# Kernel tuning notes

Hardware: AMD Instinct MI355X
Metric: run time of the kernel (lower is better)

Reference implementation:

```python
import jax, jax.numpy as jnp
import numpy as np

EPS = 1e-8
NUM_HEADS = 4


def setup_inputs() -> dict:
    key = jax.random.key(0)
    ks = jax.random.split(key, 20)
    N, D = 8192, 200      # total nodes, gnn/text dim
    B = 4                  # graphs (text batch)
    E, DEG = 4096, 16      # hyperedges, nodes per hyperedge
    H = 128                # fusion hidden dim
    f = lambda k, s: jax.random.normal(k, s, dtype=jnp.float32) * 0.05
    return {
        "x": jax.random.normal(ks[0], (N, D), dtype=jnp.float32),
        "text": jax.random.normal(ks[1], (B, D), dtype=jnp.float32),
        "W": f(ks[2], (D, D)),
        "b": jnp.zeros((D,), jnp.float32),
        "gate_w": f(ks[3], (D, 1)),
        "gate_b": jnp.zeros((1,), jnp.float32),
        "gnn_w": f(ks[4], (D, H)), "gnn_b": f(ks[5], (H,)),
        "text_w": f(ks[6], (D, H)), "text_b": f(ks[7], (H,)),
        "in_w": f(ks[8], (H, 3 * H)), "in_b": f(ks[9], (3 * H,)),
        "attn_out_w": f(ks[10], (H, H)), "attn_out_b": f(ks[11], (H,)),
        "fgate_w": f(ks[12], (2 * H, H)), "fgate_b": f(ks[13], (H,)),
        "outp_w": f(ks[14], (H, D)), "outp_b": f(ks[15], (D,)),
        "edge_nodes": jax.random.randint(ks[16], (E, DEG), 0, N),
    }


def _forward(x, text, W, b, gate_w, gate_b, gnn_w, gnn_b, text_w, text_b,
             in_w, in_b, attn_out_w, attn_out_b, fgate_w, fgate_b,
             outp_w, outp_b, edge_nodes):
    N, D = x.shape
    E, DEG = edge_nodes.shape
    # --- HypergraphConv: incidence build + normalized Laplacian propagation ---
    out = x @ W                                         # [N, D]
    # H[node, edge] = 1/len(edge); duplicates overwrite (set), as in torch loop
    Hinc = jnp.zeros((N, E), x.dtype).at[edge_nodes, jnp.arange(E)[:, None]].set(1.0 / DEG)
    Dv = Hinc.sum(axis=1)                               # node degree [N]
    De = Hinc.sum(axis=0)                               # edge degree [E]
    dv = 1.0 / jnp.sqrt(Dv + EPS)
    de = 1.0 / (De + EPS)
    Hl = Hinc * dv[:, None]                             # Dv^-1/2 H
    L = (Hl * de[None, :]) @ Hl.T                       # Dv^-1/2 H De^-1 H^T Dv^-1/2
    hyper_out = L @ out                                 # [N, D]
    alpha = jax.nn.sigmoid(x.mean(axis=0, keepdims=True) @ gate_w + gate_b)  # [1,1]
    gnn_feat = alpha * out + (1.0 - alpha) * hyper_out + b
    # --- CrossModalAttentionFusion on per-graph node features (3D path) ---
    B = text.shape[0]
    Nn = N // B
    gnn3 = gnn_feat.reshape(B, Nn, D)
    gp = gnn3 @ gnn_w + gnn_b                           # [B, Nn, H]
    tp = (text @ text_w + text_b)[:, None, :]           # [B, 1, H]
    Hd = gp.shape[-1]
    hd = Hd // NUM_HEADS
    q = gp @ in_w[:, :Hd] + in_b[:Hd]
    k = tp @ in_w[:, Hd:2 * Hd] + in_b[Hd:2 * Hd]
    v = tp @ in_w[:, 2 * Hd:] + in_b[2 * Hd:]
    qh = q.reshape(B, Nn, NUM_HEADS, hd).transpose(0, 2, 1, 3)   # [B,h,Nn,hd]
    kh = k.reshape(B, 1, NUM_HEADS, hd).transpose(0, 2, 1, 3)    # [B,h,1,hd]
    vh = v.reshape(B, 1, NUM_HEADS, hd).transpose(0, 2, 1, 3)
    scores = jnp.einsum("bhqd,bhkd->bhqk", qh, kh) / jnp.sqrt(jnp.float32(hd))
    attn = jax.nn.softmax(scores, axis=-1)              # kv_len=1 -> ones
    att = jnp.einsum("bhqk,bhkd->bhqd", attn, vh)
    att = att.transpose(0, 2, 1, 3).reshape(B, Nn, Hd) @ attn_out_w + attn_out_b
    g = jax.nn.sigmoid(jnp.concatenate([gp, att], axis=-1) @ fgate_w + fgate_b)
    fused = g * gp + (1.0 - g) * att
    return fused @ outp_w + outp_b                      # [B, Nn, D]


def reference(x, text, W, b, gate_w, gate_b, gnn_w, gnn_b, text_w, text_b,
              in_w, in_b, attn_out_w, attn_out_b, fgate_w, fgate_b,
              outp_w, outp_b, edge_nodes):
    return _forward(x, text, W, b, gate_w, gate_b, gnn_w, gnn_b, text_w, text_b,
                    in_w, in_b, attn_out_w, attn_out_b, fgate_w, fgate_b,
                    outp_w, outp_b, edge_nodes)
```

## Files before the change

kernel.cpp:

```cpp
#include <hip/hip_runtime.h>
#include <hip/hip_bf16.h>

#define NODES 8192
#define DIM   200
#define NEDGE 4096
#define DEGREE 16
#define NB    4
#define NNODE 2048
#define HD    128
#define MT    8

__global__ void k_front(const float* __restrict__ x, const int* __restrict__ en,
                        const float* __restrict__ W, const float* __restrict__ gnn_w,
                        const float* __restrict__ bias, const float* __restrict__ gnn_b,
                        const float* __restrict__ text, const float* __restrict__ text_w,
                        const float* __restrict__ text_b, const float* __restrict__ in_w,
                        const float* __restrict__ in_b, const float* __restrict__ aow,
                        const float* __restrict__ aob, const float* __restrict__ fgw,
                        const float* __restrict__ fgb, float* __restrict__ colsum,
                        int* __restrict__ cnt, int* __restrict__ emask,
                        float* __restrict__ Wg, float* __restrict__ bg,
                        float* __restrict__ attO, float* __restrict__ attg) {
    __shared__ float st[DIM];
    __shared__ float part[2][HD];
    __shared__ float vin[HD];
    int b = blockIdx.x, t = threadIdx.x;
    if (b < 256) {
        if (t < DIM) {
            float acc = 0.f;
            int r0 = b * 32;
            for (int r = 0; r < 32; r++) acc += x[(r0 + r) * DIM + t];
            atomicAdd(&colsum[t], acc);
        }
        return;
    }
    if (b < 272) {
        int e = (b - 256) * 256 + t;
        int idx[DEGREE];
#pragma unroll
        for (int i = 0; i < DEGREE; i++) idx[i] = en[e * DEGREE + i];
        int mask = 0;
#pragma unroll
        for (int i = 0; i < DEGREE; i++) {
            bool uniq = true;
            for (int j = 0; j < i; j++) uniq = uniq && (idx[j] != idx[i]);
            if (uniq) { mask |= (1 << i); atomicAdd(&cnt[idx[i]], 1); }
        }
        emask[e] = mask;
        return;
    }
    if (b < 372) {
        int r = 2 * (b - 272) + (t >> 7);
        int c = t & 127;
        const float* vec = &W[r * DIM];
        float acc = 0.f;
        for (int k = 0; k < DIM; k++) acc += vec[k] * gnn_w[k * HD + c];
        Wg[r * HD + c] = acc;
        return;
    }
    if (b == 372) {
        if (t < HD) {
            float acc = 0.f;
            for (int k = 0; k < DIM; k++) acc += bias[k] * gnn_w[k * HD + t];
            bg[t] = acc + gnn_b[t];
        }
        return;
    }
    int g = b - 373;
    int c = t & 127, h = t >> 7;
    if (t < DIM) st[t] = text[g * DIM + t];
    __syncthreads();
    {
        float acc = 0.f;
        int k0 = h * 100;
        for (int k = k0; k < k0 + 100; k++) acc += st[k] * text_w[k * HD + c];
        part[h][c] = acc;
    }
    __syncthreads();
    if (t < HD) vin[t] = part[0][t] + part[1][t] + text_b[t];
    __syncthreads();
    {
        float acc = 0.f;
        int k0 = h * 64;
        for (int k = k0; k < k0 + 64; k++) acc += vin[k] * in_w[k * 3 * HD + 2 * HD + c];
        part[h][c] = acc;
    }
    __syncthreads();
    if (t < HD) vin[t] = part[0][t] + part[1][t] + in_b[2 * HD + t];
    __syncthreads();
    {
        float acc = 0.f;
        int k0 = h * 64;
        for (int k = k0; k < k0 + 64; k++) acc += vin[k] * aow[k * HD + c];
        part[h][c] = acc;
    }
    __syncthreads();
    if (t < HD) {
        float ao = part[0][t] + part[1][t] + aob[t];
        attO[g * HD + t] = ao;
        vin[t] = ao;
    }
    __syncthreads();
    {
        float acc = 0.f;
        int k0 = h * 64;
        for (int k = k0; k < k0 + 64; k++) acc += vin[k] * fgw[(HD + k) * HD + c];
        part[h][c] = acc;
    }
    __syncthreads();
    if (t < HD) attg[g * HD + t] = part[0][t] + part[1][t] + fgb[t];
}

__global__ void k_xwg(const float* __restrict__ x, const float* __restrict__ Wg,
                      float* __restrict__ out2, const float* __restrict__ colsum,
                      const float* __restrict__ gate_w, const float* __restrict__ gate_b,
                      float* __restrict__ alpha, const int* __restrict__ cnt,
                      float* __restrict__ dv) {
    __shared__ float sx[MT * DIM];
    int t = threadIdx.x;
    if (blockIdx.x == NODES / MT) {
        __shared__ float red[256];
        red[t] = (t < DIM) ? colsum[t] * gate_w[t] : 0.f;
        __syncthreads();
        for (int o = 128; o > 0; o >>= 1) {
            if (t < o) red[t] += red[t + o];
            __syncthreads();
        }
        if (t == 0) {
            float z = red[0] / (float)NODES + gate_b[0];
            alpha[0] = 1.0f / (1.0f + expf(-z));
        }
        return;
    }
    if (blockIdx.x > NODES / MT) {
        int n = (blockIdx.x - NODES / MT - 1) * 256 + t;
        dv[n] = 1.0f / sqrtf((float)cnt[n] * (1.0f / 16.0f) + 1e-8f);
        return;
    }
    int bm = blockIdx.x * MT;
    const float4* x4 = (const float4*)(x + bm * DIM);
    float4* sx4 = (float4*)sx;
    for (int i = t; i < MT * DIM / 4; i += 256) sx4[i] = x4[i];
    __syncthreads();
    int c = t & 127, rg = t >> 7;
    float acc[4] = {0.f, 0.f, 0.f, 0.f};
    for (int k = 0; k < DIM; k++) {
        float w = Wg[k * HD + c];
#pragma unroll
        for (int i = 0; i < 4; i++) acc[i] += sx[(rg * 4 + i) * DIM + k] * w;
    }
#pragma unroll
    for (int i = 0; i < 4; i++) out2[(bm + rg * 4 + i) * HD + c] = acc[i];
}

__global__ void k_edge(const int* __restrict__ en, const int* __restrict__ emask,
                       const float* __restrict__ dv, const float* __restrict__ out2,
                       float* __restrict__ accum) {
    int e = blockIdx.x * 2 + (threadIdx.x >> 7);
    int c = threadIdx.x & 127;
    int m = emask[e];
    float De = (float)__popc(m) * (1.0f / 16.0f);
    float de = 1.0f / (De + 1e-8f);
    int nd[DEGREE];
#pragma unroll
    for (int i = 0; i < DEGREE; i++) nd[i] = en[e * DEGREE + i];
    float acc = 0.f;
#pragma unroll
    for (int i = 0; i < DEGREE; i++)
        if ((m >> i) & 1) acc += dv[nd[i]] * out2[nd[i] * HD + c];
    float s = de * acc;
#pragma unroll
    for (int i = 0; i < DEGREE; i++)
        if ((m >> i) & 1) atomicAdd(&accum[nd[i] * HD + c], s);
}

__global__ void k_tail(const float* __restrict__ out2, const float* __restrict__ accum,
                       const float* __restrict__ dv, const float* __restrict__ alpha,
                       const float* __restrict__ bg, const float* __restrict__ fgw,
                       const float* __restrict__ attO, const float* __restrict__ attg,
                       const float* __restrict__ opw, const float* __restrict__ opb,
                       float* __restrict__ out) {
    __shared__ float sgp[MT][HD];
    int bm = blockIdx.x * MT;
    int b = bm >> 11;
    int t = threadIdx.x;
    int c = t & 127, rg = t >> 7;
    float a = alpha[0];
    float bgc = bg[c];
#pragma unroll
    for (int i = 0; i < 4; i++) {
        int r = rg * 4 + i;
        int n = bm + r;
        float hyp = accum[n * HD + c] * dv[n] * (1.0f / 256.0f);
        sgp[r][c] = a * out2[n * HD + c] + (1.0f - a) * hyp + bgc;
    }
    __syncthreads();
    float ao = attO[b * HD + c];
    float ag = attg[b * HD + c];
    float acc[4] = {ag, ag, ag, ag};
    for (int j = 0; j < HD; j++) {
        float w = fgw[j * HD + c];
#pragma unroll
        for (int i = 0; i < 4; i++) acc[i] += sgp[rg * 4 + i][j] * w;
    }
    __syncthreads();
#pragma unroll
    for (int i = 0; i < 4; i++) {
        int r = rg * 4 + i;
        float g = 1.0f / (1.0f + expf(-acc[i]));
        sgp[r][c] = g * sgp[r][c] + (1.0f - g) * ao;
    }
    __syncthreads();
    if (t < DIM) {
        float accO[MT];
        float ob = opb[t];
#pragma unroll
        for (int i = 0; i < MT; i++) accO[i] = ob;
        for (int j = 0; j < HD; j++) {
            float w = opw[j * DIM + t];
#pragma unroll
            for (int i = 0; i < MT; i++) accO[i] += sgp[i][j] * w;
        }
#pragma unroll
        for (int i = 0; i < MT; i++) out[(bm + i) * DIM + t] = accO[i];
    }
}

extern "C" void kernel_launch(void* const* d_in, const int* in_sizes, int n_in,
                              void* d_out, int out_size, void* d_ws, size_t ws_size,
                              hipStream_t stream) {
    const float* x      = (const float*)d_in[0];
    const float* text   = (const float*)d_in[1];
    const float* W      = (const float*)d_in[2];
    const float* bias   = (const float*)d_in[3];
    const float* gate_w = (const float*)d_in[4];
    const float* gate_b = (const float*)d_in[5];
    const float* gnn_w  = (const float*)d_in[6];
    const float* gnn_b  = (const float*)d_in[7];
    const float* text_w = (const float*)d_in[8];
    const float* text_b = (const float*)d_in[9];
    const float* in_w   = (const float*)d_in[10];
    const float* in_b   = (const float*)d_in[11];
    const float* aow    = (const float*)d_in[12];
    const float* aob    = (const float*)d_in[13];
    const float* fgw    = (const float*)d_in[14];
    const float* fgb    = (const float*)d_in[15];
    const float* opw    = (const float*)d_in[16];
    const float* opb    = (const float*)d_in[17];
    const int*   en     = (const int*)d_in[18];
    float* out = (float*)d_out;

    char* p = (char*)d_ws;
    int*   cnt    = (int*)p;   p += NODES * sizeof(int);
    float* colsum = (float*)p; p += DIM * sizeof(float);
    float* accum  = (float*)p; p += (size_t)NODES * HD * sizeof(float);
    float* out2   = (float*)p; p += (size_t)NODES * HD * sizeof(float);
    float* Wg     = (float*)p; p += DIM * HD * sizeof(float);
    float* dv     = (float*)p; p += NODES * sizeof(float);
    float* alpha  = (float*)p; p += sizeof(float);
    float* bg     = (float*)p; p += HD * sizeof(float);
    float* attO   = (float*)p; p += NB * HD * sizeof(float);
    float* attg   = (float*)p; p += NB * HD * sizeof(float);
    int*   emask  = (int*)p;   p += NEDGE * sizeof(int);

    hipMemsetAsync(cnt, 0, (NODES + DIM + NODES * HD) * sizeof(int), stream);

    k_front<<<377, 256, 0, stream>>>(x, en, W, gnn_w, bias, gnn_b, text, text_w,
                                     text_b, in_w, in_b, aow, aob, fgw, fgb,
                                     colsum, cnt, emask, Wg, bg, attO, attg);
    k_xwg<<<NODES / MT + 1 + NODES / 256, 256, 0, stream>>>(x, Wg, out2, colsum, gate_w,
                                                            gate_b, alpha, cnt, dv);
    k_edge<<<NEDGE / 2, 256, 0, stream>>>(en, emask, dv, out2, accum);
    k_tail<<<NODES / MT, 256, 0, stream>>>(out2, accum, dv, alpha, bg, fgw,
                                           attO, attg, opw, opb, out);
}
```

Before: 185.4 us.

## Replace scatter atomics with per-node edge lists and gather in tail kernel

Builds a per-node list of incident hyperedges (capped at 32) during the uniqueness pass, then stores per-edge sums to a tE buffer instead of atomically scattering into a node accumulator. The tail kernel gathers edge sums per node through this list, and the dv array is recomputed inline from counts. This removes the large memset of accum and the float atomics in the edge kernel, at the cost of an indirect gather. Nodes with more than 32 incident edges would be silently truncated, and the order in which slots are filled by atomics is nondeterministic.

```diff
diff --git a/kernel.cpp b/kernel.cpp
--- a/kernel.cpp
+++ b/kernel.cpp
@@ -9,6 +9,11 @@
 #define NNODE 2048
 #define HD    128
 #define MT    8
+#define ECAP  32
+
+__device__ __forceinline__ float dv_of(int cnt) {
+    return 1.0f / sqrtf((float)cnt * (1.0f / 16.0f) + 1e-8f);
+}
 
 __global__ void k_front(const float* __restrict__ x, const int* __restrict__ en,
                         const float* __restrict__ W, const float* __restrict__ gnn_w,
@@ -19,8 +24,9 @@
                         const float* __restrict__ aob, const float* __restrict__ fgw,
                         const float* __restrict__ fgb, float* __restrict__ colsum,
                         int* __restrict__ cnt, int* __restrict__ emask,
-                        float* __restrict__ Wg, float* __restrict__ bg,
-                        float* __restrict__ attO, float* __restrict__ attg) {
+                        int* __restrict__ elist2, float* __restrict__ Wg,
+                        float* __restrict__ bg, float* __restrict__ attO,
+                        float* __restrict__ attg) {
     __shared__ float st[DIM];
     __shared__ float part[2][HD];
     __shared__ float vin[HD];
@@ -44,7 +50,11 @@
         for (int i = 0; i < DEGREE; i++) {
             bool uniq = true;
             for (int j = 0; j < i; j++) uniq = uniq && (idx[j] != idx[i]);
-            if (uniq) { mask |= (1 << i); atomicAdd(&cnt[idx[i]], 1); }
+            if (uniq) {
+                mask |= (1 << i);
+                int slot = atomicAdd(&cnt[idx[i]], 1);
+                if (slot < ECAP) elist2[idx[i] * ECAP + slot] = e;
+            }
         }
         emask[e] = mask;
         return;
@@ -114,8 +124,7 @@
 __global__ void k_xwg(const float* __restrict__ x, const float* __restrict__ Wg,
                       float* __restrict__ out2, const float* __restrict__ colsum,
                       const float* __restrict__ gate_w, const float* __restrict__ gate_b,
-                      float* __restrict__ alpha, const int* __restrict__ cnt,
-                      float* __restrict__ dv) {
+                      float* __restrict__ alpha) {
     __shared__ float sx[MT * DIM];
     int t = threadIdx.x;
     if (blockIdx.x == NODES / MT) {
@@ -132,11 +141,6 @@
         }
         return;
     }
-    if (blockIdx.x > NODES / MT) {
-        int n = (blockIdx.x - NODES / MT - 1) * 256 + t;
-        dv[n] = 1.0f / sqrtf((float)cnt[n] * (1.0f / 16.0f) + 1e-8f);
-        return;
-    }
     int bm = blockIdx.x * MT;
     const float4* x4 = (const float4*)(x + bm * DIM);
     float4* sx4 = (float4*)sx;
@@ -153,9 +157,9 @@
     for (int i = 0; i < 4; i++) out2[(bm + rg * 4 + i) * HD + c] = acc[i];
 }
 
-__global__ void k_edge(const int* __restrict__ en, const int* __restrict__ emask,
-                       const float* __restrict__ dv, const float* __restrict__ out2,
-                       float* __restrict__ accum) {
+__global__ void k_tE(const int* __restrict__ en, const int* __restrict__ emask,
+                     const int* __restrict__ cnt, const float* __restrict__ out2,
+                     float* __restrict__ tE) {
     int e = blockIdx.x * 2 + (threadIdx.x >> 7);
     int c = threadIdx.x & 127;
     int m = emask[e];
@@ -167,23 +171,30 @@
     float acc = 0.f;
 #pragma unroll
     for (int i = 0; i < DEGREE; i++)
-        if ((m >> i) & 1) acc += dv[nd[i]] * out2[nd[i] * HD + c];
-    float s = de * acc;
-#pragma unroll
-    for (int i = 0; i < DEGREE; i++)
-        if ((m >> i) & 1) atomicAdd(&accum[nd[i] * HD + c], s);
-}
-
-__global__ void k_tail(const float* __restrict__ out2, const float* __restrict__ accum,
-                       const float* __restrict__ dv, const float* __restrict__ alpha,
-                       const float* __restrict__ bg, const float* __restrict__ fgw,
-                       const float* __restrict__ attO, const float* __restrict__ attg,
-                       const float* __restrict__ opw, const float* __restrict__ opb,
-                       float* __restrict__ out) {
+        if ((m >> i) & 1) acc += dv_of(cnt[nd[i]]) * out2[nd[i] * HD + c];
+    tE[e * HD + c] = de * acc;
+}
+
+__global__ void k_tail(const float* __restrict__ out2, const float* __restrict__ tE,
+                       const int* __restrict__ cnt, const int* __restrict__ elist2,
+                       const float* __restrict__ alpha, const float* __restrict__ bg,
+                       const float* __restrict__ fgw, const float* __restrict__ attO,
+                       const float* __restrict__ attg, const float* __restrict__ opw,
+                       const float* __restrict__ opb, float* __restrict__ out) {
     __shared__ float sgp[MT][HD];
+    __shared__ int   sid[MT][ECAP];
+    __shared__ int   scount[MT];
     int bm = blockIdx.x * MT;
     int b = bm >> 11;
     int t = threadIdx.x;
+    {
+        int r = t >> 5, sl = t & 31;
+        int n = bm + r;
+        int cc = cnt[n]; cc = cc < ECAP ? cc : ECAP;
+        if (sl == 0) scount[r] = cc;
+        if (sl < cc) sid[r][sl] = elist2[n * ECAP + sl];
+    }
+    __syncthreads();
     int c = t & 127, rg = t >> 7;
     float a = alpha[0];
     float bgc = bg[c];
@@ -191,7 +202,10 @@
     for (int i = 0; i < 4; i++) {
         int r = rg * 4 + i;
         int n = bm + r;
-        float hyp = accum[n * HD + c] * dv[n] * (1.0f / 256.0f);
+        int cc = scount[r];
+        float hyp = 0.f;
+        for (int j = 0; j < cc; j++) hyp += tE[sid[r][j] * HD + c];
+        hyp *= dv_of(cnt[n]) * (1.0f / 256.0f);
         sgp[r][c] = a * out2[n * HD + c] + (1.0f - a) * hyp + bgc;
     }
     __syncthreads();
@@ -253,24 +267,23 @@
     char* p = (char*)d_ws;
     int*   cnt    = (int*)p;   p += NODES * sizeof(int);
     float* colsum = (float*)p; p += DIM * sizeof(float);
-    float* accum  = (float*)p; p += (size_t)NODES * HD * sizeof(float);
     float* out2   = (float*)p; p += (size_t)NODES * HD * sizeof(float);
+    float* tE     = (float*)p; p += (size_t)NEDGE * HD * sizeof(float);
+    int*   elist2 = (int*)p;   p += (size_t)NODES * ECAP * sizeof(int);
     float* Wg     = (float*)p; p += DIM * HD * sizeof(float);
-    float* dv     = (float*)p; p += NODES * sizeof(float);
     float* alpha  = (float*)p; p += sizeof(float);
     float* bg     = (float*)p; p += HD * sizeof(float);
     float* attO   = (float*)p; p += NB * HD * sizeof(float);
     float* attg   = (float*)p; p += NB * HD * sizeof(float);
     int*   emask  = (int*)p;   p += NEDGE * sizeof(int);
 
-    hipMemsetAsync(cnt, 0, (NODES + DIM + NODES * HD) * sizeof(int), stream);
+    hipMemsetAsync(cnt, 0, (NODES + DIM) * sizeof(int), stream);
 
     k_front<<<377, 256, 0, stream>>>(x, en, W, gnn_w, bias, gnn_b, text, text_w,
                                      text_b, in_w, in_b, aow, aob, fgw, fgb,
-                                     colsum, cnt, emask, Wg, bg, attO, attg);
-    k_xwg<<<NODES / MT + 1 + NODES / 256, 256, 0, stream>>>(x, Wg, out2, colsum, gate_w,
-                                                            gate_b, alpha, cnt, dv);
-    k_edge<<<NEDGE / 2, 256, 0, stream>>>(en, emask, dv, out2, accum);
-    k_tail<<<NODES / MT, 256, 0, stream>>>(out2, accum, dv, alpha, bg, fgw,
+                                     colsum, cnt, emask, elist2, Wg, bg, attO, attg);
+    k_xwg<<<NODES / MT + 1, 256, 0, stream>>>(x, Wg, out2, colsum, gate_w, gate_b, alpha);
+    k_tE<<<NEDGE / 2, 256, 0, stream>>>(en, emask, cnt, out2, tE);
+    k_tail<<<NODES / MT, 256, 0, stream>>>(out2, tE, cnt, elist2, alpha, bg, fgw,
                                            attO, attg, opw, opb, out);
 }
```

Result: faster. 167.6 us (-9.6%).
